# Kernel tuning notes

Measured on AMD Instinct MI355X. Metric: run time of the kernel, lower is better.

Reference implementation:

```python
import jax, jax.numpy as jnp
import numpy as np

H_DIM = 256
N_HEADS = 8
HEAD_DIM = H_DIM // N_HEADS
B, N = 2, 2048
LN_EPS = 1e-5


def setup_inputs() -> dict:
    key = jax.random.key(0)
    ks = jax.random.split(key, 20)
    s = 1.0 / np.sqrt(H_DIM)
    inp = {
        'hidden': jax.random.normal(ks[0], (B, N, H_DIM), jnp.float32),
        'adjacency': jax.random.uniform(ks[1], (B, N, N), jnp.float32),
        'positions': jax.random.uniform(ks[2], (B, N, 2), jnp.float32),
        # linear weights stored as (in, out): y = x @ W + b
        'wq': jax.random.normal(ks[3], (H_DIM, H_DIM), jnp.float32) * s,
        'bq': jnp.zeros((H_DIM,), jnp.float32),
        'wk': jax.random.normal(ks[4], (H_DIM, H_DIM), jnp.float32) * s,
        'bk': jnp.zeros((H_DIM,), jnp.float32),
        'wv': jax.random.normal(ks[5], (H_DIM, H_DIM), jnp.float32) * s,
        'bv': jnp.zeros((H_DIM,), jnp.float32),
        'wo': jax.random.normal(ks[6], (H_DIM, H_DIM), jnp.float32) * s,
        'bo': jnp.zeros((H_DIM,), jnp.float32),
        'g1': jnp.ones((H_DIM,), jnp.float32),
        'b1': jnp.zeros((H_DIM,), jnp.float32),
        'g2': jnp.ones((H_DIM,), jnp.float32),
        'b2': jnp.zeros((H_DIM,), jnp.float32),
        'w_ff1': jax.random.normal(ks[7], (H_DIM, 4 * H_DIM), jnp.float32) * s,
        'b_ff1': jnp.zeros((4 * H_DIM,), jnp.float32),
        'w_ff2': jax.random.normal(ks[8], (4 * H_DIM, H_DIM), jnp.float32) * (1.0 / np.sqrt(4 * H_DIM)),
        'b_ff2': jnp.zeros((H_DIM,), jnp.float32),
    }
    return inp


def _layernorm(x, g, b):
    mu = jnp.mean(x, axis=-1, keepdims=True)
    var = jnp.var(x, axis=-1, keepdims=True)
    return (x - mu) * jax.lax.rsqrt(var + LN_EPS) * g + b


def reference(hidden, adjacency, positions, wq, bq, wk, bk, wv, bv, wo, bo,
              g1, b1, g2, b2, w_ff1, b_ff1, w_ff2, b_ff2):
    b_, n_, _ = hidden.shape
    normalized = _layernorm(hidden, g1, b1)
    # project and split heads: [B, H, N, Dh]
    def heads(x):
        return x.reshape(b_, n_, N_HEADS, HEAD_DIM).transpose(0, 2, 1, 3)
    q = heads(normalized @ wq + bq)
    k = heads(normalized @ wk + bk)
    v = heads(normalized @ wv + bv)
    logits = jnp.einsum('bhnd,bhmd->bhnm', q, k) / np.sqrt(HEAD_DIM)
    cond = adjacency[:, None, :, :]  # mode == 'connectivity'
    logits = logits + (2.0 * cond - 1.0)
    weights = jax.nn.softmax(logits, axis=-1)
    weights = weights * (0.25 + 0.75 * cond)
    weights = weights / jnp.maximum(weights.sum(axis=-1, keepdims=True), 1e-6)
    attended = jnp.einsum('bhnm,bhmd->bhnd', weights, v)
    attended = attended.transpose(0, 2, 1, 3).reshape(b_, n_, H_DIM)
    hidden = hidden + attended @ wo + bo
    h2 = _layernorm(hidden, g2, b2)
    ff = jax.nn.gelu(h2 @ w_ff1 + b_ff1, approximate=False) @ w_ff2 + b_ff2
    return hidden + ff
```

## Files before the change

kernel.cpp:

```cpp
#include <hip/hip_runtime.h>
#include <math.h>

#define BB 2
#define NN 2048
#define HD 256
#define NH 8
#define DH 32
#define NTOK (BB*NN)
#define QKVLD 768
#define NSPLIT 4

typedef _Float16 h8 __attribute__((ext_vector_type(8)));
typedef _Float16 h4 __attribute__((ext_vector_type(4)));
typedef float fx4 __attribute__((ext_vector_type(4)));

#define LOG2E 1.4426950408889634f
#define SQ_LOG2 0.25503486f

__global__ __launch_bounds__(256) void ln_kernel(const float* __restrict__ x,
    const float* __restrict__ g, const float* __restrict__ bta,
    _Float16* __restrict__ yh)
{
  int row  = blockIdx.x * 4 + (threadIdx.x >> 6);
  int lane = threadIdx.x & 63;
  const float* xr = x + (size_t)row * HD + lane * 4;
  float4 v = *(const float4*)xr;
  float s = v.x + v.y + v.z + v.w;
  #pragma unroll
  for (int off = 32; off > 0; off >>= 1) s += __shfl_xor(s, off);
  float mu = s * (1.0f / HD);
  float dx0 = v.x - mu, dx1 = v.y - mu, dx2 = v.z - mu, dx3 = v.w - mu;
  float ss = dx0*dx0 + dx1*dx1 + dx2*dx2 + dx3*dx3;
  #pragma unroll
  for (int off = 32; off > 0; off >>= 1) ss += __shfl_xor(ss, off);
  float rinv = rsqrtf(ss * (1.0f / HD) + 1e-5f);
  float4 gv = *(const float4*)(g   + lane * 4);
  float4 bv = *(const float4*)(bta + lane * 4);
  float o[4];
  o[0] = dx0 * rinv * gv.x + bv.x;
  o[1] = dx1 * rinv * gv.y + bv.y;
  o[2] = dx2 * rinv * gv.z + bv.z;
  o[3] = dx3 * rinv * gv.w + bv.w;
  h4 hh;
  #pragma unroll
  for (int j = 0; j < 4; j++) hh[j] = (_Float16)o[j];
  *(h4*)(yh + (size_t)row * HD + lane * 4) = hh;
}

__device__ __forceinline__ void do_transpose(const float* __restrict__ W,
    _Float16* __restrict__ Wh, int Nw, int rowoff, int ldout, float scale,
    int bx, int by, float (*tile)[33])
{
  int k0 = by * 32, n0 = bx * 32;
  int c = threadIdx.x & 31, r = threadIdx.x >> 5;
  #pragma unroll
  for (int i = 0; i < 4; i++)
    tile[r + i * 8][c] = W[(size_t)(k0 + r + i * 8) * Nw + n0 + c];
  __syncthreads();
  #pragma unroll
  for (int i = 0; i < 4; i++) {
    int n = r + i * 8;
    Wh[(size_t)(rowoff + n0 + n) * ldout + k0 + c] = (_Float16)(tile[c][n] * scale);
  }
}

__global__ __launch_bounds__(256) void prep_kernel(
    const float* wq, const float* wk, const float* wv, const float* wo,
    const float* wf1, const float* wf2,
    const float* bq, const float* bk, const float* bv,
    _Float16* WtQKVh, _Float16* WtOh, _Float16* WtF1h, _Float16* WtF2h,
    float* biasqkv)
{
  __shared__ float tile[32][33];
  int bid = blockIdx.x;
  if (bid < 64)        do_transpose(wq,  WtQKVh,  256,   0,  256, SQ_LOG2, bid & 7, bid >> 3, tile);
  else if (bid < 128)  do_transpose(wk,  WtQKVh,  256, 256,  256, 1.0f, (bid-64) & 7, (bid-64) >> 3, tile);
  else if (bid < 192)  do_transpose(wv,  WtQKVh,  256, 512,  256, 1.0f, (bid-128) & 7, (bid-128) >> 3, tile);
  else if (bid < 256)  do_transpose(wo,  WtOh,    256,   0,  256, 1.0f, (bid-192) & 7, (bid-192) >> 3, tile);
  else if (bid < 512)  do_transpose(wf1, WtF1h,  1024,   0,  256, 1.0f, (bid-256) & 31, (bid-256) >> 5, tile);
  else if (bid < 768)  do_transpose(wf2, WtF2h,   256,   0, 1024, 1.0f, (bid-512) & 7, (bid-512) >> 3, tile);
  else {
    #pragma unroll
    for (int j = 0; j < 3; j++) {
      int t = j * 256 + threadIdx.x;
      biasqkv[t] = (t < 256) ? bq[t] * SQ_LOG2 : (t < 512) ? bk[t - 256] : bv[t - 512];
    }
  }
}

template<int KK, int NT, int NX, int ACT, int RES, int OM>
__global__ __launch_bounds__(256) void gemm16_kernel(
    const _Float16* __restrict__ Ah, const _Float16* __restrict__ Wh,
    const float* __restrict__ bias, const float* __restrict__ resid,
    float* __restrict__ Cf, _Float16* __restrict__ Ch,
    _Float16* __restrict__ vtb, int N)
{
  const int lin = blockIdx.x;
  const int qch = gridDim.x >> 3;
  const int wg = (lin & 7) * qch + (lin >> 3);
  const int bx = wg % NX, by = wg / NX;
  const int n0 = bx * (NT * 16);
  const int m0 = by * 64;
  const int t = threadIdx.x, w = t >> 6, l = t & 63;
  const int ml = l & 15, g = l >> 4;
  const int mrow = m0 + w * 16 + ml;

  const _Float16* aph = Ah + (size_t)mrow * KK + g * 8;
  const _Float16* whp[NT];
  #pragma unroll
  for (int nt = 0; nt < NT; nt++)
    whp[nt] = Wh + (size_t)(n0 + nt * 16 + ml) * KK + g * 8;

  fx4 acc[NT];
  #pragma unroll
  for (int nt = 0; nt < NT; nt++) acc[nt] = (fx4){0.f, 0.f, 0.f, 0.f};

  #pragma unroll 4
  for (int k0 = 0; k0 < KK; k0 += 32) {
    h8 ah = *(const h8*)(aph + k0);
    #pragma unroll
    for (int nt = 0; nt < NT; nt++) {
      h8 wh = *(const h8*)(whp[nt] + k0);
      acc[nt] = __builtin_amdgcn_mfma_f32_16x16x32_f16(ah, wh, acc[nt], 0, 0, 0);
    }
  }

  #pragma unroll
  for (int nt = 0; nt < NT; nt++) {
    int n = n0 + nt * 16 + ml;
    float bv = bias[n];
    #pragma unroll
    for (int i = 0; i < 4; i++) {
      int m = m0 + w * 16 + 4 * g + i;
      float vv = acc[nt][i] + bv;
      if (ACT == 1) vv = 0.5f * vv * (1.0f + erff(vv * 0.70710678118654752f));
      if (RES)      vv += resid[(size_t)m * N + n];
      if (OM == 0) {
        Cf[(size_t)m * N + n] = vv;
      } else if (OM == 1) {
        Ch[(size_t)m * N + n] = (_Float16)vv;
      } else {
        if (n < 512) Ch[(size_t)m * QKVLD + n] = (_Float16)vv;
        else {
          int dim = n - 512, kv = m & (NN - 1), bb = m >> 11;
          int kvp = (kv & ~31) | ((kv & 15) << 1) | ((kv >> 4) & 1);
          vtb[((size_t)(bb * HD + dim)) * NN + kvp] = (_Float16)vv;
        }
      }
    }
  }
}

__global__ __launch_bounds__(256) void attn_mfma_kernel(
    const _Float16* __restrict__ qkv16, const _Float16* __restrict__ vtb,
    const float* __restrict__ adj,
    _Float16* __restrict__ Opart, float* __restrict__ Mpart, float* __restrict__ Spart)
{
  __shared__ _Float16 Ksh[2][64][40];
  __shared__ _Float16 Vp[2][32][72];

  const int z = blockIdx.z;
  const int b = z >> 2, quarter = z & 3;
  const int h = blockIdx.y;
  const int q0 = blockIdx.x * 64;
  const int t = threadIdx.x;
  const int w = t >> 6, l = t & 63;
  const int m = l & 15, g = l >> 4;
  const int kvbase = quarter * (NN / NSPLIT);
  const int NTILES = NN / NSPLIT / 64;

  const int qrow = q0 + w * 16 + m;
  h8 qh = *(const h8*)(qkv16 + ((size_t)(b * NN + qrow)) * QKVLD + h * DH + g * 8);

  fx4 ot0 = {0.f, 0.f, 0.f, 0.f};
  fx4 ot1 = {0.f, 0.f, 0.f, 0.f};
  float M = -3.0e38f, S = 0.0f;

  const float* adjrow = adj + ((size_t)(b * NN + qrow)) * NN + kvbase;

  const int krow = t >> 2, kd0 = (t & 3) * 8;
  const int vdim = t >> 3, vkc = (t & 7) * 8;
  const _Float16* kbase = qkv16 + ((size_t)(b * NN + kvbase + krow)) * QKVLD + 256 + h * DH + kd0;
  const _Float16* vbase = vtb + ((size_t)(b * HD + h * DH + vdim)) * NN + kvbase + vkc;

  h8 kreg = *(const h8*)kbase;
  h8 vreg = *(const h8*)vbase;
  float4 adjreg[4];
  #pragma unroll
  for (int p = 0; p < 4; p++) adjreg[p] = *(const float4*)(adjrow + p * 16 + g * 4);

  *(h8*)&Ksh[0][krow][kd0] = kreg;
  *(h8*)&Vp[0][vdim][vkc]  = vreg;
  kreg = *(const h8*)(kbase + (size_t)64 * QKVLD);
  vreg = *(const h8*)(vbase + 64);
  __syncthreads();

  for (int tt = 0; tt < NTILES; ++tt) {
    const int cur = tt & 1;
    float4 a4[4];
    #pragma unroll
    for (int p = 0; p < 4; p++) a4[p] = adjreg[p];
    if (tt + 1 < NTILES) {
      #pragma unroll
      for (int p = 0; p < 4; p++)
        adjreg[p] = *(const float4*)(adjrow + (tt + 1) * 64 + p * 16 + g * 4);
    }

    h8 kh0 = *(const h8*)&Ksh[cur][     m][g * 8];
    h8 kh1 = *(const h8*)&Ksh[cur][16 + m][g * 8];
    h8 kh2 = *(const h8*)&Ksh[cur][32 + m][g * 8];
    h8 kh3 = *(const h8*)&Ksh[cur][48 + m][g * 8];
    fx4 z4 = {0.f, 0.f, 0.f, 0.f};
    fx4 st[4];
    st[0] = __builtin_amdgcn_mfma_f32_16x16x32_f16(kh0, qh, z4, 0, 0, 0);
    st[1] = __builtin_amdgcn_mfma_f32_16x16x32_f16(kh1, qh, z4, 0, 0, 0);
    st[2] = __builtin_amdgcn_mfma_f32_16x16x32_f16(kh2, qh, z4, 0, 0, 0);
    st[3] = __builtin_amdgcn_mfma_f32_16x16x32_f16(kh3, qh, z4, 0, 0, 0);

    float lv[16];
    #pragma unroll
    for (int p = 0; p < 4; p++) {
      const float* ap = (const float*)&a4[p];
      #pragma unroll
      for (int i = 0; i < 4; i++)
        lv[p * 4 + i] = st[p][i] + (2.0f * LOG2E) * ap[i] - LOG2E;
    }
    float x8[8];
    #pragma unroll
    for (int i = 0; i < 8; i++) x8[i] = fmaxf(lv[i], lv[i + 8]);
    float x4[4];
    #pragma unroll
    for (int i = 0; i < 4; i++) x4[i] = fmaxf(x8[i], x8[i + 4]);
    float lmax = fmaxf(fmaxf(x4[0], x4[1]), fmaxf(x4[2], x4[3]));
    if (!__all(lmax <= M + 8.0f)) {
      float rmax = fmaxf(lmax, __shfl_xor(lmax, 16));
      rmax = fmaxf(rmax, __shfl_xor(rmax, 32));
      float mnew = fmaxf(M, rmax);
      float resc = __builtin_amdgcn_exp2f(M - mnew);
      S *= resc; ot0 *= resc; ot1 *= resc;
      M = mnew;
    }
    #pragma unroll
    for (int p = 0; p < 4; p++) {
      const float* ap = (const float*)&a4[p];
      #pragma unroll
      for (int i = 0; i < 4; i++) {
        float e = __builtin_amdgcn_exp2f(lv[p * 4 + i] - M);
        float pp = (0.25f + 0.75f * ap[i]) * e;
        lv[p * 4 + i] = pp;
        S += pp;
      }
    }
    h8 ph0, ph1;
    #pragma unroll
    for (int q2 = 0; q2 < 4; q2++) {
      ph0[2*q2]     = (_Float16)lv[q2];
      ph0[2*q2 + 1] = (_Float16)lv[4 + q2];
      ph1[2*q2]     = (_Float16)lv[8 + q2];
      ph1[2*q2 + 1] = (_Float16)lv[12 + q2];
    }

    h8 v00 = *(const h8*)&Vp[cur][m][g * 8];
    h8 v01 = *(const h8*)&Vp[cur][m][32 + g * 8];
    h8 v10 = *(const h8*)&Vp[cur][16 + m][g * 8];
    h8 v11 = *(const h8*)&Vp[cur][16 + m][32 + g * 8];
    ot0 = __builtin_amdgcn_mfma_f32_16x16x32_f16(v00, ph0, ot0, 0, 0, 0);
    ot0 = __builtin_amdgcn_mfma_f32_16x16x32_f16(v01, ph1, ot0, 0, 0, 0);
    ot1 = __builtin_amdgcn_mfma_f32_16x16x32_f16(v10, ph0, ot1, 0, 0, 0);
    ot1 = __builtin_amdgcn_mfma_f32_16x16x32_f16(v11, ph1, ot1, 0, 0, 0);

    if (tt + 1 < NTILES) {
      *(h8*)&Ksh[cur ^ 1][krow][kd0] = kreg;
      *(h8*)&Vp[cur ^ 1][vdim][vkc]  = vreg;
      if (tt + 2 < NTILES) {
        kreg = *(const h8*)(kbase + (size_t)((tt + 2) * 64) * QKVLD);
        vreg = *(const h8*)(vbase + (tt + 2) * 64);
      }
    }
    __syncthreads();
  }

  S += __shfl_xor(S, 16);
  S += __shfl_xor(S, 32);

  float is = 1.0f / S;
  size_t prow = ((size_t)(z * NH + h)) * NN + qrow;
  _Float16* po = Opart + prow * 32;
  h4 o0h, o1h;
  #pragma unroll
  for (int j = 0; j < 4; j++) {
    o0h[j] = (_Float16)(ot0[j] * is);
    o1h[j] = (_Float16)(ot1[j] * is);
  }
  *(h4*)(po + 4 * g)      = o0h;
  *(h4*)(po + 16 + 4 * g) = o1h;
  if (g == 0) { Mpart[prow] = M; Spart[prow] = S; }
}

__global__ __launch_bounds__(256) void attn_combine_kernel(
    const _Float16* __restrict__ Opart, const float* __restrict__ Mpart,
    const float* __restrict__ Spart, _Float16* __restrict__ atth)
{
  int idx = blockIdx.x * 256 + threadIdx.x;
  int dg  = idx & 7;
  int rowid = idx >> 3;
  int qrow = rowid & (NN - 1);
  int bh = rowid >> 11;
  int b = bh >> 3, h = bh & 7;
  size_t p[NSPLIT];
  float mz[NSPLIT], sz[NSPLIT];
  float mm = -3.0e38f;
  #pragma unroll
  for (int zq = 0; zq < NSPLIT; zq++) {
    p[zq] = ((size_t)((b * NSPLIT + zq) * NH + h)) * NN + qrow;
    mz[zq] = Mpart[p[zq]];
    sz[zq] = Spart[p[zq]];
    mm = fmaxf(mm, mz[zq]);
  }
  float den = 0.f;
  float wz[NSPLIT];
  #pragma unroll
  for (int zq = 0; zq < NSPLIT; zq++) {
    wz[zq] = sz[zq] * __builtin_amdgcn_exp2f(mz[zq] - mm);
    den += wz[zq];
  }
  float is = 1.0f / den;
  float ov[4] = {0.f, 0.f, 0.f, 0.f};
  #pragma unroll
  for (int zq = 0; zq < NSPLIT; zq++) {
    h4 o = *(const h4*)(Opart + p[zq] * 32 + dg * 4);
    float wzz = wz[zq] * is;
    #pragma unroll
    for (int j = 0; j < 4; j++) ov[j] += wzz * (float)o[j];
  }
  h4 hh;
  #pragma unroll
  for (int j = 0; j < 4; j++) hh[j] = (_Float16)ov[j];
  *(h4*)(atth + ((size_t)(b * NN + qrow)) * HD + h * DH + dg * 4) = hh;
}

extern "C" void kernel_launch(void* const* d_in, const int* in_sizes, int n_in,
                              void* d_out, int out_size, void* d_ws, size_t ws_size,
                              hipStream_t stream)
{
  const float* hidden    = (const float*)d_in[0];
  const float* adjacency = (const float*)d_in[1];
  const float* wq  = (const float*)d_in[3];
  const float* bq  = (const float*)d_in[4];
  const float* wk  = (const float*)d_in[5];
  const float* bk  = (const float*)d_in[6];
  const float* wv  = (const float*)d_in[7];
  const float* bv  = (const float*)d_in[8];
  const float* wo  = (const float*)d_in[9];
  const float* bo  = (const float*)d_in[10];
  const float* g1  = (const float*)d_in[11];
  const float* b1  = (const float*)d_in[12];
  const float* g2  = (const float*)d_in[13];
  const float* b2  = (const float*)d_in[14];
  const float* wf1 = (const float*)d_in[15];
  const float* bf1 = (const float*)d_in[16];
  const float* wf2 = (const float*)d_in[17];
  const float* bf2 = (const float*)d_in[18];
  float* out = (float*)d_out;

  char* base = (char*)d_ws;
  const size_t MB = 1024 * 1024;
  _Float16* norm1h = (_Float16*)(base);
  _Float16* qkv16  = (_Float16*)(base + 4*MB);
  _Float16* vtb    = (_Float16*)(base + 10*MB);
  _Float16* atth   = (_Float16*)(base + 12*MB);
  float*    hid2   = (float*)(base + 16*MB);
  _Float16* Opart = (_Float16*)(base + 20*MB);
  _Float16* ffah  = (_Float16*)(base + 20*MB);
  float* Mpart = (float*)(base + 36*MB);
  float* Spart = (float*)(base + 36*MB + 512*1024);
  _Float16* wtb = (_Float16*)(base + 37*MB);
  _Float16* WtQKVh = wtb; wtb += 768 * 256;
  _Float16* WtOh   = wtb; wtb += 256 * 256;
  _Float16* WtF1h  = wtb; wtb += 1024 * 256;
  _Float16* WtF2h  = wtb; wtb += 256 * 1024;
  float* biasqkv = (float*)(base + 40*MB);

  prep_kernel<<<769, 256, 0, stream>>>(wq, wk, wv, wo, wf1, wf2, bq, bk, bv,
      WtQKVh, WtOh, WtF1h, WtF2h, biasqkv);

  ln_kernel<<<NTOK / 4, 256, 0, stream>>>(hidden, g1, b1, norm1h);

  gemm16_kernel<256, 4, 12, 0, 0, 2><<<768, 256, 0, stream>>>(
      norm1h, WtQKVh, biasqkv, nullptr, nullptr, qkv16, vtb, QKVLD);

  attn_mfma_kernel<<<dim3(NN / 64, NH, BB * NSPLIT), 256, 0, stream>>>(
      qkv16, vtb, adjacency, Opart, Mpart, Spart);
  attn_combine_kernel<<<(BB * NH * NN * 8) / 256, 256, 0, stream>>>(
      Opart, Mpart, Spart, atth);

  gemm16_kernel<256, 2, 8, 0, 1, 0><<<512, 256, 0, stream>>>(
      atth, WtOh, bo, hidden, hid2, nullptr, nullptr, 256);

  ln_kernel<<<NTOK / 4, 256, 0, stream>>>(hid2, g2, b2, norm1h);

  gemm16_kernel<256, 4, 16, 1, 0, 1><<<1024, 256, 0, stream>>>(
      norm1h, WtF1h, bf1, nullptr, nullptr, ffah, nullptr, 1024);

  gemm16_kernel<1024, 2, 8, 0, 1, 0><<<512, 256, 0, stream>>>(
      ffah, WtF2h, bf2, hid2, out, nullptr, nullptr, 256);
}
```

Before: 132.0 us.

## Restructure attention so each block shares adjacency across four heads

Each block now processes four heads (one per wave) for 64 query rows, so waves in a block read identical adjacency rows and reuse each K/V tile across four query subtiles. The KV split is raised to 8 and the grid is reshaped to match. The cross-iteration prefetch and block-wide double buffering are dropped in favour of per-wave LDS tiles with no barriers, which exposes global load latency. More partial outputs go to the combine step, and workspace offsets are compacted.

```diff
diff --git a/kernel.cpp b/kernel.cpp
--- a/kernel.cpp
+++ b/kernel.cpp
@@ -8,7 +8,9 @@
 #define DH 32
 #define NTOK (BB*NN)
 #define QKVLD 768
-#define NSPLIT 4
+#define NSPLIT 8
+#define KVPB (NN/NSPLIT)
+#define NTILES (KVPB/64)
 
 typedef _Float16 h8 __attribute__((ext_vector_type(8)));
 typedef _Float16 h4 __attribute__((ext_vector_type(4)));
@@ -151,150 +153,155 @@
   }
 }
 
-__global__ __launch_bounds__(256) void attn_mfma_kernel(
+__global__ __launch_bounds__(256, 4) void attn_mfma_kernel(
     const _Float16* __restrict__ qkv16, const _Float16* __restrict__ vtb,
     const float* __restrict__ adj,
     _Float16* __restrict__ Opart, float* __restrict__ Mpart, float* __restrict__ Spart)
 {
-  __shared__ _Float16 Ksh[2][64][40];
-  __shared__ _Float16 Vp[2][32][72];
-
-  const int z = blockIdx.z;
-  const int b = z >> 2, quarter = z & 3;
-  const int h = blockIdx.y;
+  __shared__ _Float16 Ksh[4][64][40];
+  __shared__ _Float16 Vp[4][32][72];
+
+  const int zz = blockIdx.y;
+  const int b  = zz >> 4;
+  const int hg = (zz >> 3) & 1;
+  const int e  = zz & 7;
   const int q0 = blockIdx.x * 64;
   const int t = threadIdx.x;
   const int w = t >> 6, l = t & 63;
+  const int h = hg * 4 + w;
   const int m = l & 15, g = l >> 4;
-  const int kvbase = quarter * (NN / NSPLIT);
-  const int NTILES = NN / NSPLIT / 64;
-
-  const int qrow = q0 + w * 16 + m;
-  h8 qh = *(const h8*)(qkv16 + ((size_t)(b * NN + qrow)) * QKVLD + h * DH + g * 8);
-
-  fx4 ot0 = {0.f, 0.f, 0.f, 0.f};
-  fx4 ot1 = {0.f, 0.f, 0.f, 0.f};
-  float M = -3.0e38f, S = 0.0f;
-
-  const float* adjrow = adj + ((size_t)(b * NN + qrow)) * NN + kvbase;
-
-  const int krow = t >> 2, kd0 = (t & 3) * 8;
-  const int vdim = t >> 3, vkc = (t & 7) * 8;
-  const _Float16* kbase = qkv16 + ((size_t)(b * NN + kvbase + krow)) * QKVLD + 256 + h * DH + kd0;
-  const _Float16* vbase = vtb + ((size_t)(b * HD + h * DH + vdim)) * NN + kvbase + vkc;
-
-  h8 kreg = *(const h8*)kbase;
-  h8 vreg = *(const h8*)vbase;
-  float4 adjreg[4];
-  #pragma unroll
-  for (int p = 0; p < 4; p++) adjreg[p] = *(const float4*)(adjrow + p * 16 + g * 4);
-
-  *(h8*)&Ksh[0][krow][kd0] = kreg;
-  *(h8*)&Vp[0][vdim][vkc]  = vreg;
-  kreg = *(const h8*)(kbase + (size_t)64 * QKVLD);
-  vreg = *(const h8*)(vbase + 64);
-  __syncthreads();
+  const int kvbase = e * KVPB;
+
+  h8 qh[4];
+  #pragma unroll
+  for (int qs = 0; qs < 4; qs++)
+    qh[qs] = *(const h8*)(qkv16 + ((size_t)(b * NN + q0 + qs * 16 + m)) * QKVLD + h * DH + g * 8);
+
+  fx4 ot[4][2];
+  float M[4], S[4];
+  #pragma unroll
+  for (int qs = 0; qs < 4; qs++) {
+    ot[qs][0] = (fx4){0.f, 0.f, 0.f, 0.f};
+    ot[qs][1] = (fx4){0.f, 0.f, 0.f, 0.f};
+    M[qs] = -3.0e38f; S[qs] = 0.f;
+  }
+
+  const _Float16* kgb = qkv16 + ((size_t)(b * NN + kvbase)) * QKVLD + 256 + (size_t)h * DH;
+  const _Float16* vgb = vtb + ((size_t)(b * HD + h * DH)) * NN + kvbase;
 
   for (int tt = 0; tt < NTILES; ++tt) {
-    const int cur = tt & 1;
-    float4 a4[4];
-    #pragma unroll
-    for (int p = 0; p < 4; p++) a4[p] = adjreg[p];
-    if (tt + 1 < NTILES) {
-      #pragma unroll
-      for (int p = 0; p < 4; p++)
-        adjreg[p] = *(const float4*)(adjrow + (tt + 1) * 64 + p * 16 + g * 4);
-    }
-
-    h8 kh0 = *(const h8*)&Ksh[cur][     m][g * 8];
-    h8 kh1 = *(const h8*)&Ksh[cur][16 + m][g * 8];
-    h8 kh2 = *(const h8*)&Ksh[cur][32 + m][g * 8];
-    h8 kh3 = *(const h8*)&Ksh[cur][48 + m][g * 8];
-    fx4 z4 = {0.f, 0.f, 0.f, 0.f};
-    fx4 st[4];
-    st[0] = __builtin_amdgcn_mfma_f32_16x16x32_f16(kh0, qh, z4, 0, 0, 0);
-    st[1] = __builtin_amdgcn_mfma_f32_16x16x32_f16(kh1, qh, z4, 0, 0, 0);
-    st[2] = __builtin_amdgcn_mfma_f32_16x16x32_f16(kh2, qh, z4, 0, 0, 0);
-    st[3] = __builtin_amdgcn_mfma_f32_16x16x32_f16(kh3, qh, z4, 0, 0, 0);
-
-    float lv[16];
-    #pragma unroll
-    for (int p = 0; p < 4; p++) {
-      const float* ap = (const float*)&a4[p];
-      #pragma unroll
-      for (int i = 0; i < 4; i++)
-        lv[p * 4 + i] = st[p][i] + (2.0f * LOG2E) * ap[i] - LOG2E;
-    }
-    float x8[8];
-    #pragma unroll
-    for (int i = 0; i < 8; i++) x8[i] = fmaxf(lv[i], lv[i + 8]);
-    float x4[4];
-    #pragma unroll
-    for (int i = 0; i < 4; i++) x4[i] = fmaxf(x8[i], x8[i + 4]);
-    float lmax = fmaxf(fmaxf(x4[0], x4[1]), fmaxf(x4[2], x4[3]));
-    if (!__all(lmax <= M + 8.0f)) {
-      float rmax = fmaxf(lmax, __shfl_xor(lmax, 16));
-      rmax = fmaxf(rmax, __shfl_xor(rmax, 32));
-      float mnew = fmaxf(M, rmax);
-      float resc = __builtin_amdgcn_exp2f(M - mnew);
-      S *= resc; ot0 *= resc; ot1 *= resc;
-      M = mnew;
-    }
-    #pragma unroll
-    for (int p = 0; p < 4; p++) {
-      const float* ap = (const float*)&a4[p];
+    #pragma unroll
+    for (int it = 0; it < 4; it++) {
+      int c = it * 64 + l;
+      int krow = c >> 2, kseg = (c & 3) * 8;
+      h8 kx = *(const h8*)(kgb + (size_t)(tt * 64 + krow) * QKVLD + kseg);
+      *(h8*)&Ksh[w][krow][kseg] = kx;
+    }
+    #pragma unroll
+    for (int it = 0; it < 4; it++) {
+      int c = it * 64 + l;
+      int vdim = c >> 3, vseg = (c & 7) * 8;
+      h8 vx = *(const h8*)(vgb + (size_t)vdim * NN + tt * 64 + vseg);
+      *(h8*)&Vp[w][vdim][vseg] = vx;
+    }
+
+    h8 kh0 = *(const h8*)&Ksh[w][     m][g * 8];
+    h8 kh1 = *(const h8*)&Ksh[w][16 + m][g * 8];
+    h8 kh2 = *(const h8*)&Ksh[w][32 + m][g * 8];
+    h8 kh3 = *(const h8*)&Ksh[w][48 + m][g * 8];
+    h8 v00 = *(const h8*)&Vp[w][m][g * 8];
+    h8 v01 = *(const h8*)&Vp[w][m][32 + g * 8];
+    h8 v10 = *(const h8*)&Vp[w][16 + m][g * 8];
+    h8 v11 = *(const h8*)&Vp[w][16 + m][32 + g * 8];
+
+    #pragma unroll
+    for (int qs = 0; qs < 4; qs++) {
+      const float* ar = adj + ((size_t)(b * NN + q0 + qs * 16 + m)) * NN + kvbase + tt * 64;
+      float4 a0 = *(const float4*)(ar + g * 4);
+      float4 a1 = *(const float4*)(ar + 16 + g * 4);
+      float4 a2 = *(const float4*)(ar + 32 + g * 4);
+      float4 a3 = *(const float4*)(ar + 48 + g * 4);
+
+      fx4 z4 = {0.f, 0.f, 0.f, 0.f};
+      fx4 st0 = __builtin_amdgcn_mfma_f32_16x16x32_f16(kh0, qh[qs], z4, 0, 0, 0);
+      fx4 st1 = __builtin_amdgcn_mfma_f32_16x16x32_f16(kh1, qh[qs], z4, 0, 0, 0);
+      fx4 st2 = __builtin_amdgcn_mfma_f32_16x16x32_f16(kh2, qh[qs], z4, 0, 0, 0);
+      fx4 st3 = __builtin_amdgcn_mfma_f32_16x16x32_f16(kh3, qh[qs], z4, 0, 0, 0);
+
+      float lv[16];
+      const float* a0p = (const float*)&a0;
+      const float* a1p = (const float*)&a1;
+      const float* a2p = (const float*)&a2;
+      const float* a3p = (const float*)&a3;
       #pragma unroll
       for (int i = 0; i < 4; i++) {
-        float e = __builtin_amdgcn_exp2f(lv[p * 4 + i] - M);
-        float pp = (0.25f + 0.75f * ap[i]) * e;
-        lv[p * 4 + i] = pp;
-        S += pp;
+        lv[i]      = st0[i] + (2.0f * LOG2E) * a0p[i] - LOG2E;
+        lv[4 + i]  = st1[i] + (2.0f * LOG2E) * a1p[i] - LOG2E;
+        lv[8 + i]  = st2[i] + (2.0f * LOG2E) * a2p[i] - LOG2E;
+        lv[12 + i] = st3[i] + (2.0f * LOG2E) * a3p[i] - LOG2E;
       }
-    }
-    h8 ph0, ph1;
-    #pragma unroll
-    for (int q2 = 0; q2 < 4; q2++) {
-      ph0[2*q2]     = (_Float16)lv[q2];
-      ph0[2*q2 + 1] = (_Float16)lv[4 + q2];
-      ph1[2*q2]     = (_Float16)lv[8 + q2];
-      ph1[2*q2 + 1] = (_Float16)lv[12 + q2];
-    }
-
-    h8 v00 = *(const h8*)&Vp[cur][m][g * 8];
-    h8 v01 = *(const h8*)&Vp[cur][m][32 + g * 8];
-    h8 v10 = *(const h8*)&Vp[cur][16 + m][g * 8];
-    h8 v11 = *(const h8*)&Vp[cur][16 + m][32 + g * 8];
-    ot0 = __builtin_amdgcn_mfma_f32_16x16x32_f16(v00, ph0, ot0, 0, 0, 0);
-    ot0 = __builtin_amdgcn_mfma_f32_16x16x32_f16(v01, ph1, ot0, 0, 0, 0);
-    ot1 = __builtin_amdgcn_mfma_f32_16x16x32_f16(v10, ph0, ot1, 0, 0, 0);
-    ot1 = __builtin_amdgcn_mfma_f32_16x16x32_f16(v11, ph1, ot1, 0, 0, 0);
-
-    if (tt + 1 < NTILES) {
-      *(h8*)&Ksh[cur ^ 1][krow][kd0] = kreg;
-      *(h8*)&Vp[cur ^ 1][vdim][vkc]  = vreg;
-      if (tt + 2 < NTILES) {
-        kreg = *(const h8*)(kbase + (size_t)((tt + 2) * 64) * QKVLD);
-        vreg = *(const h8*)(vbase + (tt + 2) * 64);
+      float x8[8];
+      #pragma unroll
+      for (int i = 0; i < 8; i++) x8[i] = fmaxf(lv[i], lv[i + 8]);
+      float x4[4];
+      #pragma unroll
+      for (int i = 0; i < 4; i++) x4[i] = fmaxf(x8[i], x8[i + 4]);
+      float lmax = fmaxf(fmaxf(x4[0], x4[1]), fmaxf(x4[2], x4[3]));
+      if (!__all(lmax <= M[qs] + 8.0f)) {
+        float rmax = fmaxf(lmax, __shfl_xor(lmax, 16));
+        rmax = fmaxf(rmax, __shfl_xor(rmax, 32));
+        float mnew = fmaxf(M[qs], rmax);
+        float resc = __builtin_amdgcn_exp2f(M[qs] - mnew);
+        S[qs] *= resc; ot[qs][0] *= resc; ot[qs][1] *= resc;
+        M[qs] = mnew;
       }
-    }
-    __syncthreads();
-  }
-
-  S += __shfl_xor(S, 16);
-  S += __shfl_xor(S, 32);
-
-  float is = 1.0f / S;
-  size_t prow = ((size_t)(z * NH + h)) * NN + qrow;
-  _Float16* po = Opart + prow * 32;
-  h4 o0h, o1h;
-  #pragma unroll
-  for (int j = 0; j < 4; j++) {
-    o0h[j] = (_Float16)(ot0[j] * is);
-    o1h[j] = (_Float16)(ot1[j] * is);
-  }
-  *(h4*)(po + 4 * g)      = o0h;
-  *(h4*)(po + 16 + 4 * g) = o1h;
-  if (g == 0) { Mpart[prow] = M; Spart[prow] = S; }
+      float sacc = S[qs];
+      #pragma unroll
+      for (int p = 0; p < 4; p++) {
+        const float* ap = (p == 0) ? a0p : (p == 1) ? a1p : (p == 2) ? a2p : a3p;
+        #pragma unroll
+        for (int i = 0; i < 4; i++) {
+          float ee = __builtin_amdgcn_exp2f(lv[p * 4 + i] - M[qs]);
+          float pp = (0.25f + 0.75f * ap[i]) * ee;
+          lv[p * 4 + i] = pp;
+          sacc += pp;
+        }
+      }
+      S[qs] = sacc;
+      h8 ph0, ph1;
+      #pragma unroll
+      for (int q2 = 0; q2 < 4; q2++) {
+        ph0[2 * q2]     = (_Float16)lv[q2];
+        ph0[2 * q2 + 1] = (_Float16)lv[4 + q2];
+        ph1[2 * q2]     = (_Float16)lv[8 + q2];
+        ph1[2 * q2 + 1] = (_Float16)lv[12 + q2];
+      }
+      ot[qs][0] = __builtin_amdgcn_mfma_f32_16x16x32_f16(v00, ph0, ot[qs][0], 0, 0, 0);
+      ot[qs][0] = __builtin_amdgcn_mfma_f32_16x16x32_f16(v01, ph1, ot[qs][0], 0, 0, 0);
+      ot[qs][1] = __builtin_amdgcn_mfma_f32_16x16x32_f16(v10, ph0, ot[qs][1], 0, 0, 0);
+      ot[qs][1] = __builtin_amdgcn_mfma_f32_16x16x32_f16(v11, ph1, ot[qs][1], 0, 0, 0);
+    }
+  }
+
+  const int ps = b * NSPLIT + e;
+  #pragma unroll
+  for (int qs = 0; qs < 4; qs++) {
+    float Sq = S[qs];
+    Sq += __shfl_xor(Sq, 16);
+    Sq += __shfl_xor(Sq, 32);
+    float is = 1.0f / Sq;
+    size_t prow = ((size_t)(ps * NH + h)) * NN + (q0 + qs * 16 + m);
+    _Float16* po = Opart + prow * 32;
+    h4 o0h, o1h;
+    #pragma unroll
+    for (int j = 0; j < 4; j++) {
+      o0h[j] = (_Float16)(ot[qs][0][j] * is);
+      o1h[j] = (_Float16)(ot[qs][1][j] * is);
+    }
+    *(h4*)(po + 4 * g)      = o0h;
+    *(h4*)(po + 16 + 4 * g) = o1h;
+    if (g == 0) { Mpart[prow] = M[qs]; Spart[prow] = Sq; }
+  }
 }
 
 __global__ __launch_bounds__(256) void attn_combine_kernel(
@@ -366,20 +373,20 @@
   char* base = (char*)d_ws;
   const size_t MB = 1024 * 1024;
   _Float16* norm1h = (_Float16*)(base);
-  _Float16* qkv16  = (_Float16*)(base + 4*MB);
-  _Float16* vtb    = (_Float16*)(base + 10*MB);
-  _Float16* atth   = (_Float16*)(base + 12*MB);
-  float*    hid2   = (float*)(base + 16*MB);
-  _Float16* Opart = (_Float16*)(base + 20*MB);
-  _Float16* ffah  = (_Float16*)(base + 20*MB);
-  float* Mpart = (float*)(base + 36*MB);
-  float* Spart = (float*)(base + 36*MB + 512*1024);
-  _Float16* wtb = (_Float16*)(base + 37*MB);
+  _Float16* qkv16  = (_Float16*)(base + 2*MB);
+  _Float16* vtb    = (_Float16*)(base + 8*MB);
+  _Float16* atth   = (_Float16*)(base + 10*MB);
+  float*    hid2   = (float*)(base + 12*MB);
+  _Float16* Opart = (_Float16*)(base + 16*MB);
+  _Float16* ffah  = (_Float16*)(base + 16*MB);
+  float* Mpart = (float*)(base + 33*MB);
+  float* Spart = (float*)(base + 34*MB);
+  _Float16* wtb = (_Float16*)(base + 35*MB);
   _Float16* WtQKVh = wtb; wtb += 768 * 256;
   _Float16* WtOh   = wtb; wtb += 256 * 256;
   _Float16* WtF1h  = wtb; wtb += 1024 * 256;
   _Float16* WtF2h  = wtb; wtb += 256 * 1024;
-  float* biasqkv = (float*)(base + 40*MB);
+  float* biasqkv = (float*)(base + 37*MB);
 
   prep_kernel<<<769, 256, 0, stream>>>(wq, wk, wv, wo, wf1, wf2, bq, bk, bv,
       WtQKVh, WtOh, WtF1h, WtF2h, biasqkv);
@@ -389,7 +396,7 @@
   gemm16_kernel<256, 4, 12, 0, 0, 2><<<768, 256, 0, stream>>>(
       norm1h, WtQKVh, biasqkv, nullptr, nullptr, qkv16, vtb, QKVLD);
 
-  attn_mfma_kernel<<<dim3(NN / 64, NH, BB * NSPLIT), 256, 0, stream>>>(
+  attn_mfma_kernel<<<dim3(NN / 64, BB * 2 * NSPLIT), 256, 0, stream>>>(
       qkv16, vtb, adjacency, Opart, Mpart, Spart);
   attn_combine_kernel<<<(BB * NH * NN * 8) / 256, 256, 0, stream>>>(
       Opart, Mpart, Spart, atth);
```

New measurement: 192.9 us. 1.46x slower.
